# Kernel tuning notes

Measured on AMD Instinct MI355X. Metric: run time of the kernel, lower is better.

The kernel has to match this reference:

```python
import jax, jax.numpy as jnp
import numpy as np

N_EMBED = 1024
N_HEADS = 16
HEAD = N_EMBED // N_HEADS
EPS = 1e-5


def setup_inputs() -> dict:
    key = jax.random.key(0)
    ks = jax.random.split(key, 16)
    C = N_EMBED
    s = lambda fan_in: 1.0 / np.sqrt(fan_in)
    return {
        "x": jax.random.normal(ks[0], (4, 2048, C), jnp.float32),
        "ln1_g": jnp.ones((C,), jnp.float32),
        "ln1_b": jnp.zeros((C,), jnp.float32),
        "w_attn": jax.random.normal(ks[1], (C, 3 * C), jnp.float32) * s(C),
        "b_attn": jnp.zeros((3 * C,), jnp.float32),
        "w_proj": jax.random.normal(ks[2], (C, C), jnp.float32) * s(C),
        "b_proj": jnp.zeros((C,), jnp.float32),
        "ln2_g": jnp.ones((C,), jnp.float32),
        "ln2_b": jnp.zeros((C,), jnp.float32),
        "w_fc": jax.random.normal(ks[3], (C, 4 * C), jnp.float32) * s(C),
        "b_fc": jnp.zeros((4 * C,), jnp.float32),
        "w_fc2": jax.random.normal(ks[4], (4 * C, C), jnp.float32) * s(4 * C),
        "b_fc2": jnp.zeros((C,), jnp.float32),
    }


def _layernorm(x, g, b):
    mu = jnp.mean(x, axis=-1, keepdims=True)
    var = jnp.mean(jnp.square(x - mu), axis=-1, keepdims=True)
    return (x - mu) * jax.lax.rsqrt(var + EPS) * g + b


def _attention(x, w_attn, b_attn, w_proj, b_proj):
    B, T, C = x.shape
    qkv = x @ w_attn + b_attn  # [B,T,3C]
    q, k, v = jnp.split(qkv, 3, axis=-1)
    q = q.reshape(B, T, N_HEADS, HEAD).transpose(0, 2, 1, 3)  # [B,H,T,D]
    k = k.reshape(B, T, N_HEADS, HEAD).transpose(0, 2, 1, 3)
    v = v.reshape(B, T, N_HEADS, HEAD).transpose(0, 2, 1, 3)
    scale = 1.0 / np.sqrt(HEAD)
    affin = jnp.einsum("bhqd,bhkd->bhqk", q, k) * scale  # [B,H,T,T]
    causal = jnp.tril(jnp.ones((T, T), bool))
    affin = jnp.where(causal, affin, -jnp.inf)
    affin = jax.nn.softmax(affin, axis=-1)
    y = jnp.einsum("bhqk,bhkd->bhqd", affin, v)  # [B,H,T,D]
    y = y.transpose(0, 2, 1, 3).reshape(B, T, C)
    return y @ w_proj + b_proj


def reference(x, ln1_g, ln1_b, w_attn, b_attn, w_proj, b_proj,
              ln2_g, ln2_b, w_fc, b_fc, w_fc2, b_fc2):
    x = x + _attention(_layernorm(x, ln1_g, ln1_b), w_attn, b_attn, w_proj, b_proj)
    h = _layernorm(x, ln2_g, ln2_b)
    h = jax.nn.gelu(h @ w_fc + b_fc, approximate=True)  # tanh GELU
    x = x + (h @ w_fc2 + b_fc2)
    return x
```

## Files before the change

### kernel.cpp

```cpp
#include <hip/hip_runtime.h>
#include <math.h>


#define M_ROWS 8192
#define T_SEQ 2048
#define N_EMB 1024
#define N_HEADS 16
#define HEAD_D 64

typedef _Float16 f16;
typedef __attribute__((ext_vector_type(8))) _Float16 f16x8;
typedef __attribute__((ext_vector_type(4))) _Float16 f16x4;
typedef __attribute__((ext_vector_type(4))) float f32x4;

__device__ __forceinline__ void async16(void* lds, const void* g) {
    __builtin_amdgcn_global_load_lds(
        (const __attribute__((address_space(1))) unsigned int*)g,
        (__attribute__((address_space(3))) unsigned int*)lds, 16, 0, 0);
}

__device__ __forceinline__ float gelu_tanh(float v) {
    float u = 0.7978845608028654f * (v + 0.044715f * v * v * v);
    float e = __expf(2.0f * u);
    float t = 1.0f - 2.0f / (e + 1.0f);
    return 0.5f * v * (1.0f + t);
}

__launch_bounds__(256)
__global__ void wconv_kernel(const float* __restrict__ W, f16* __restrict__ WT,
                             int K, int N) {
    __shared__ float t[32][33];
    int tx = threadIdx.x & 31, ty = threadIdx.x >> 5;
    int n0 = blockIdx.x * 32, k0 = blockIdx.y * 32;
    #pragma unroll
    for (int r = 0; r < 4; r++)
        t[ty * 4 + r][tx] = W[(size_t)(k0 + ty * 4 + r) * N + n0 + tx];
    __syncthreads();
    #pragma unroll
    for (int r = 0; r < 4; r++)
        WT[(size_t)(n0 + ty * 4 + r) * K + k0 + tx] = (f16)t[tx][ty * 4 + r];
}

__launch_bounds__(256)
__global__ void ln_kernel(const float* __restrict__ x, const float* __restrict__ g,
                          const float* __restrict__ b, f16* __restrict__ y) {
    int row = blockIdx.x;
    int tid = threadIdx.x;
    const float* xr = x + (size_t)row * N_EMB;
    float4 v = *(const float4*)(xr + tid * 4);
    float s  = v.x + v.y + v.z + v.w;
    float sq = v.x * v.x + v.y * v.y + v.z * v.z + v.w * v.w;
    #pragma unroll
    for (int off = 32; off > 0; off >>= 1) {
        s  += __shfl_down(s, off);
        sq += __shfl_down(sq, off);
    }
    __shared__ float ws_[4], wq_[4];
    __shared__ float mean_s, rstd_s;
    int lane = tid & 63, wid = tid >> 6;
    if (lane == 0) { ws_[wid] = s; wq_[wid] = sq; }
    __syncthreads();
    if (tid == 0) {
        float st = ws_[0] + ws_[1] + ws_[2] + ws_[3];
        float qt = wq_[0] + wq_[1] + wq_[2] + wq_[3];
        float mu = st * (1.0f / N_EMB);
        float var = qt * (1.0f / N_EMB) - mu * mu;
        mean_s = mu;
        rstd_s = rsqrtf(var + 1e-5f);
    }
    __syncthreads();
    float mu = mean_s, r = rstd_s;
    float4 gv = *(const float4*)(g + tid * 4);
    float4 bv = *(const float4*)(b + tid * 4);
    f16x4 o;
    o.x = (f16)((v.x - mu) * r * gv.x + bv.x);
    o.y = (f16)((v.y - mu) * r * gv.y + bv.y);
    o.z = (f16)((v.z - mu) * r * gv.z + bv.z);
    o.w = (f16)((v.w - mu) * r * gv.w + bv.w);
    *(f16x4*)(y + (size_t)row * N_EMB + tid * 4) = o;
}

template <int EPI>
__launch_bounds__(256)
__global__ void gemm_f16(const f16* __restrict__ A, const f16* __restrict__ Bt,
                         const float* __restrict__ bias, const float* __restrict__ res,
                         float* __restrict__ Cf, f16* __restrict__ Ch,
                         f16* __restrict__ vT, int K, int N) {
    __shared__ f16 As[2][128 * 32];
    __shared__ f16 Bs[2][128 * 32];
    int tid = threadIdx.x;
    int lane = tid & 63, wave = tid >> 6;
    int wr = wave >> 1, wc = wave & 1;
    int quad = lane >> 4, l16 = lane & 15;
    int m0 = blockIdx.y * 128, n0 = blockIdx.x * 128;

    int r0 = tid >> 2;
    int s0 = (tid & 3) * 8;
    const f16* paA0 = A  + (size_t)(m0 + r0) * K + s0;
    const f16* paA1 = A  + (size_t)(m0 + r0 + 64) * K + s0;
    const f16* paB0 = Bt + (size_t)(n0 + r0) * K + s0;
    const f16* paB1 = Bt + (size_t)(n0 + r0 + 64) * K + s0;
    char* dA0 = (char*)As + (size_t)tid * 16;
    char* dA1 = (char*)As + (size_t)(256 + tid) * 16;
    char* dB0 = (char*)Bs + (size_t)tid * 16;
    char* dB1 = (char*)Bs + (size_t)(256 + tid) * 16;

    async16(dA0, paA0);
    async16(dA1, paA1);
    async16(dB0, paB0);
    async16(dB1, paB1);

    f32x4 acc[4][4] = {};
    int p = 0;
    for (int k0 = 0; k0 < K; k0 += 32, p ^= 1) {
        __syncthreads();
        if (k0 + 32 < K) {
            int koff = k0 + 32;
            async16(dA0 + (p ^ 1) * 8192, paA0 + koff);
            async16(dA1 + (p ^ 1) * 8192, paA1 + koff);
            async16(dB0 + (p ^ 1) * 8192, paB0 + koff);
            async16(dB1 + (p ^ 1) * 8192, paB1 + koff);
        }
        const f16* as = As[p];
        const f16* bs = Bs[p];
        f16x8 af[4], bf[4];
        #pragma unroll
        for (int i = 0; i < 4; i++)
            af[i] = *(const f16x8*)&as[(wr * 64 + i * 16 + l16) * 32 + quad * 8];
        #pragma unroll
        for (int j = 0; j < 4; j++)
            bf[j] = *(const f16x8*)&bs[(wc * 64 + j * 16 + l16) * 32 + quad * 8];
        #pragma unroll
        for (int i = 0; i < 4; i++)
            #pragma unroll
            for (int j = 0; j < 4; j++)
                acc[i][j] = __builtin_amdgcn_mfma_f32_16x16x32_f16(
                    af[i], bf[j], acc[i][j], 0, 0, 0);
    }

    #pragma unroll
    for (int i = 0; i < 4; i++) {
        int row0 = m0 + wr * 64 + i * 16 + quad * 4;
        #pragma unroll
        for (int j = 0; j < 4; j++) {
            int col = n0 + wc * 64 + j * 16 + l16;
            float bb = bias[col];
            if (EPI == 3) {
                if (n0 < 2048) {
                    #pragma unroll
                    for (int r = 0; r < 4; r++)
                        Ch[(size_t)(row0 + r) * 2048 + col] = (f16)(acc[i][j][r] + bb);
                } else {
                    int hh = (col - 2048) >> 6, dd = col & 63;
                    int bb_ = row0 >> 11, t0 = row0 & 2047;
                    f16x4 pk;
                    pk.x = (f16)(acc[i][j][0] + bb);
                    pk.y = (f16)(acc[i][j][1] + bb);
                    pk.z = (f16)(acc[i][j][2] + bb);
                    pk.w = (f16)(acc[i][j][3] + bb);
                    *(f16x4*)(vT + ((size_t)(bb_ * 16 + hh) * 64 + dd) * 2048 + t0) = pk;
                }
            } else {
                #pragma unroll
                for (int r = 0; r < 4; r++) {
                    size_t idx = (size_t)(row0 + r) * N + col;
                    float v = acc[i][j][r] + bb;
                    if (EPI == 1) v += res[idx];
                    if (EPI == 2) Ch[idx] = (f16)gelu_tanh(v);
                    else          Cf[idx] = v;
                }
            }
        }
    }
}

__launch_bounds__(256, 2)
__global__ void flash_kernel(const f16* __restrict__ qk, const f16* __restrict__ vT,
                             f16* __restrict__ y) {
    __shared__ __align__(16) char smem[67584];
    f16* Ks = (f16*)smem;
    f16* Vs = (f16*)(smem + 16384);
    int tid = threadIdx.x;
    int lane = tid & 63, w = tid >> 6;
    int quad = lane >> 4, l16 = lane & 15;
    f16* Ps = (f16*)(smem + 32768 + w * 8704);

    int bh = blockIdx.y;
    int b = bh >> 4, h = bh & 15;

    for (int half = 0; half < 2; half++) {
        int qt = half ? (int)blockIdx.x : 15 - (int)blockIdx.x;
        int q0 = qt * 128;

        f16x8 qf[2][2];
        #pragma unroll
        for (int qn = 0; qn < 2; qn++) {
            int q = q0 + w * 32 + qn * 16 + l16;
            #pragma unroll
            for (int dblk = 0; dblk < 2; dblk++) {
                f16x8 t = *(const f16x8*)(qk + (size_t)(b * T_SEQ + q) * 2048 +
                                          h * 64 + dblk * 32 + quad * 8);
                #pragma unroll
                for (int e = 0; e < 8; e++) t[e] = t[e] * (f16)0.125f;
                qf[qn][dblk] = t;
            }
        }

        float m_r[2] = {-INFINITY, -INFINITY};
        float l_r[2] = {0.0f, 0.0f};
        f32x4 Oacc[2][4] = {};

        for (int jt = 0; jt <= qt; jt++) {
            int j0 = jt * 128;
            __syncthreads();
            #pragma unroll
            for (int i = 0; i < 4; i++) {
                int L = i * 256 + tid;
                int j = L >> 3, g1 = L & 7;
                int g = g1 ^ (j & 7);
                async16((char*)Ks + (size_t)L * 16,
                        qk + (size_t)(b * T_SEQ + j0 + j) * 2048 + 1024 + h * 64 + g * 8);
            }
            #pragma unroll
            for (int i = 0; i < 4; i++) {
                int L = i * 256 + tid;
                int d = L >> 4, g1 = L & 15;
                int g = (g1 & 8) | ((g1 ^ d) & 7);
                async16((char*)Vs + (size_t)L * 16,
                        vT + ((size_t)(bh) * 64 + d) * 2048 + j0 + g * 8);
            }
            __syncthreads();

            f32x4 S[8][2];
            #pragma unroll
            for (int jm = 0; jm < 8; jm++) {
                f16x8 kf[2];
                #pragma unroll
                for (int dblk = 0; dblk < 2; dblk++) {
                    int j = jm * 16 + l16;
                    int g = (dblk * 4 + quad) ^ (j & 7);
                    kf[dblk] = *(const f16x8*)(Ks + (size_t)(j * 8 + g) * 8);
                }
                #pragma unroll
                for (int qn = 0; qn < 2; qn++) {
                    f32x4 s = {};
                    s = __builtin_amdgcn_mfma_f32_16x16x32_f16(kf[0], qf[qn][0], s, 0, 0, 0);
                    s = __builtin_amdgcn_mfma_f32_16x16x32_f16(kf[1], qf[qn][1], s, 0, 0, 0);
                    S[jm][qn] = s;
                }
            }

            if (jt == qt) {
                #pragma unroll
                for (int jm = 0; jm < 8; jm++)
                    #pragma unroll
                    for (int qn = 0; qn < 2; qn++)
                        #pragma unroll
                        for (int r = 0; r < 4; r++) {
                            int jl = jm * 16 + quad * 4 + r;
                            int ql = w * 32 + qn * 16 + l16;
                            if (jl > ql) S[jm][qn][r] = -1e30f;
                        }
            }

            float alpha[2];
            #pragma unroll
            for (int qn = 0; qn < 2; qn++) {
                float tmax = -INFINITY;
                #pragma unroll
                for (int jm = 0; jm < 8; jm++)
                    #pragma unroll
                    for (int r = 0; r < 4; r++)
                        tmax = fmaxf(tmax, S[jm][qn][r]);
                tmax = fmaxf(tmax, __shfl_xor(tmax, 16));
                tmax = fmaxf(tmax, __shfl_xor(tmax, 32));
                float mnew = fmaxf(m_r[qn], tmax);
                alpha[qn] = __expf(m_r[qn] - mnew);
                m_r[qn] = mnew;
                float rsum = 0.0f;
                #pragma unroll
                for (int jm = 0; jm < 8; jm++)
                    #pragma unroll
                    for (int r = 0; r < 4; r++) {
                        float p = __expf(S[jm][qn][r] - mnew);
                        S[jm][qn][r] = p;
                        rsum += p;
                    }
                rsum += __shfl_xor(rsum, 16);
                rsum += __shfl_xor(rsum, 32);
                l_r[qn] = l_r[qn] * alpha[qn] + rsum;
            }

            #pragma unroll
            for (int jm = 0; jm < 8; jm++)
                #pragma unroll
                for (int qn = 0; qn < 2; qn++) {
                    f16x4 pk;
                    pk.x = (f16)S[jm][qn][0];
                    pk.y = (f16)S[jm][qn][1];
                    pk.z = (f16)S[jm][qn][2];
                    pk.w = (f16)S[jm][qn][3];
                    *(f16x4*)(Ps + (size_t)(qn * 16 + l16) * 136 + jm * 16 + quad * 4) = pk;
                }

            float aPV[2][4];
            #pragma unroll
            for (int m = 0; m < 2; m++)
                #pragma unroll
                for (int r = 0; r < 4; r++)
                    aPV[m][r] = __shfl(alpha[m], quad * 20 + r);
            #pragma unroll
            for (int m = 0; m < 2; m++)
                #pragma unroll
                for (int n = 0; n < 4; n++)
                    #pragma unroll
                    for (int r = 0; r < 4; r++)
                        Oacc[m][n][r] *= aPV[m][r];

            #pragma unroll
            for (int kblk = 0; kblk < 4; kblk++) {
                f16x8 pf[2];
                #pragma unroll
                for (int m = 0; m < 2; m++)
                    pf[m] = *(const f16x8*)(Ps + (size_t)(m * 16 + l16) * 136 +
                                            kblk * 32 + quad * 8);
                f16x8 vf[4];
                #pragma unroll
                for (int n = 0; n < 4; n++) {
                    int d = n * 16 + l16;
                    int g = (kblk * 4 + quad);
                    int gs = (g & 8) | ((g ^ d) & 7);
                    vf[n] = *(const f16x8*)(Vs + (size_t)(d * 16 + gs) * 8);
                }
                #pragma unroll
                for (int m = 0; m < 2; m++)
                    #pragma unroll
                    for (int n = 0; n < 4; n++)
                        Oacc[m][n] = __builtin_amdgcn_mfma_f32_16x16x32_f16(
                            pf[m], vf[n], Oacc[m][n], 0, 0, 0);
            }
        }

        #pragma unroll
        for (int m = 0; m < 2; m++) {
            float lPV[4];
            #pragma unroll
            for (int r = 0; r < 4; r++)
                lPV[r] = 1.0f / __shfl(l_r[m], quad * 20 + r);
            #pragma unroll
            for (int n = 0; n < 4; n++) {
                #pragma unroll
                for (int r = 0; r < 4; r++) {
                    int q = q0 + w * 32 + m * 16 + quad * 4 + r;
                    y[(size_t)(b * T_SEQ + q) * N_EMB + h * 64 + n * 16 + l16] =
                        (f16)(Oacc[m][n][r] * lPV[r]);
                }
            }
        }
    }
}

extern "C" void kernel_launch(void* const* d_in, const int* in_sizes, int n_in,
                              void* d_out, int out_size, void* d_ws, size_t ws_size,
                              hipStream_t stream) {
    const float* x      = (const float*)d_in[0];
    const float* ln1_g  = (const float*)d_in[1];
    const float* ln1_b  = (const float*)d_in[2];
    const float* w_attn = (const float*)d_in[3];
    const float* b_attn = (const float*)d_in[4];
    const float* w_proj = (const float*)d_in[5];
    const float* b_proj = (const float*)d_in[6];
    const float* ln2_g  = (const float*)d_in[7];
    const float* ln2_b  = (const float*)d_in[8];
    const float* w_fc   = (const float*)d_in[9];
    const float* b_fc   = (const float*)d_in[10];
    const float* w_fc2  = (const float*)d_in[11];
    const float* b_fc2  = (const float*)d_in[12];
    float* out = (float*)d_out;

    const size_t MB = 1024 * 1024;
    char* ws = (char*)d_ws;
    f16*   lnbuf = (f16*)ws;
    f16*   qkbuf = (f16*)(ws + 16 * MB);
    f16*   vTbuf = (f16*)(ws + 48 * MB);
    f16*   ybuf  = (f16*)(ws + 64 * MB);
    f16*   h     = (f16*)(ws + 80 * MB);
    f16*   wT    = (f16*)(ws + 144 * MB);
    f16* wT_attn = wT;
    f16* wT_proj = wT_attn + (size_t)3072 * 1024;
    f16* wT_fc   = wT_proj + (size_t)1024 * 1024;
    f16* wT_fc2  = wT_fc   + (size_t)1024 * 4096;

    wconv_kernel<<<dim3(3072 / 32, 1024 / 32), 256, 0, stream>>>(w_attn, wT_attn, 1024, 3072);
    wconv_kernel<<<dim3(1024 / 32, 1024 / 32), 256, 0, stream>>>(w_proj, wT_proj, 1024, 1024);
    wconv_kernel<<<dim3(4096 / 32, 1024 / 32), 256, 0, stream>>>(w_fc,   wT_fc,   1024, 4096);
    wconv_kernel<<<dim3(1024 / 32, 4096 / 32), 256, 0, stream>>>(w_fc2,  wT_fc2,  4096, 1024);

    ln_kernel<<<M_ROWS, 256, 0, stream>>>(x, ln1_g, ln1_b, lnbuf);
    gemm_f16<3><<<dim3(3072 / 128, M_ROWS / 128), 256, 0, stream>>>(
        lnbuf, wT_attn, b_attn, nullptr, nullptr, qkbuf, vTbuf, 1024, 3072);
    flash_kernel<<<dim3(8, 64), 256, 0, stream>>>(qkbuf, vTbuf, ybuf);
    gemm_f16<1><<<dim3(1024 / 128, M_ROWS / 128), 256, 0, stream>>>(
        ybuf, wT_proj, b_proj, x, out, nullptr, nullptr, 1024, 1024);
    ln_kernel<<<M_ROWS, 256, 0, stream>>>(out, ln2_g, ln2_b, lnbuf);
    gemm_f16<2><<<dim3(4096 / 128, M_ROWS / 128), 256, 0, stream>>>(
        lnbuf, wT_fc, b_fc, nullptr, nullptr, h, nullptr, 1024, 4096);
    gemm_f16<1><<<dim3(1024 / 128, M_ROWS / 128), 256, 0, stream>>>(
        h, wT_fc2, b_fc2, out, out, nullptr, nullptr, 4096, 1024);
}
```

Baseline: 525.3 us.

## Triple-buffer GEMM LDS pipeline with explicit vmcnt waits and XCD tile swizzle

The GEMM main loop moves from a double-buffered async global-to-LDS prefetch to a three-stage ring. Explicit s_waitcnt vmcnt values let two tiles stay in flight while the current one is consumed, and barriers now sit on both sides of the compute. Workgroup IDs are remapped so that consecutive tiles land on the same XCD for L2 reuse, and s_setprio raises wave priority during the MFMA block. The swizzle assumes the workgroup count is divisible by 8, and the extra LDS buffer plus second barrier may lower occupancy.

```diff
diff --git a/kernel.cpp b/kernel.cpp
--- a/kernel.cpp
+++ b/kernel.cpp
@@ -86,13 +86,19 @@
                          const float* __restrict__ bias, const float* __restrict__ res,
                          float* __restrict__ Cf, f16* __restrict__ Ch,
                          f16* __restrict__ vT, int K, int N) {
-    __shared__ f16 As[2][128 * 32];
-    __shared__ f16 Bs[2][128 * 32];
+    __shared__ f16 As[3][128 * 32];
+    __shared__ f16 Bs[3][128 * 32];
     int tid = threadIdx.x;
     int lane = tid & 63, wave = tid >> 6;
     int wr = wave >> 1, wc = wave & 1;
     int quad = lane >> 4, l16 = lane & 15;
-    int m0 = blockIdx.y * 128, n0 = blockIdx.x * 128;
+
+    int nx = gridDim.x;
+    int nwg = nx * gridDim.y;
+    int orig = blockIdx.y * nx + blockIdx.x;
+    int cpx = nwg >> 3;
+    int swz = (orig & 7) * cpx + (orig >> 3);
+    int m0 = (swz / nx) * 128, n0 = (swz % nx) * 128;
 
     int r0 = tid >> 2;
     int s0 = (tid & 3) * 8;
@@ -100,29 +106,39 @@
     const f16* paA1 = A  + (size_t)(m0 + r0 + 64) * K + s0;
     const f16* paB0 = Bt + (size_t)(n0 + r0) * K + s0;
     const f16* paB1 = Bt + (size_t)(n0 + r0 + 64) * K + s0;
-    char* dA0 = (char*)As + (size_t)tid * 16;
-    char* dA1 = (char*)As + (size_t)(256 + tid) * 16;
-    char* dB0 = (char*)Bs + (size_t)tid * 16;
-    char* dB1 = (char*)Bs + (size_t)(256 + tid) * 16;
-
-    async16(dA0, paA0);
-    async16(dA1, paA1);
-    async16(dB0, paB0);
-    async16(dB1, paB1);
+    char* sA0 = (char*)As + (size_t)tid * 16;
+    char* sA1 = (char*)As + (size_t)(256 + tid) * 16;
+    char* sB0 = (char*)Bs + (size_t)tid * 16;
+    char* sB1 = (char*)Bs + (size_t)(256 + tid) * 16;
+
+    int nt = K >> 5;
+
+    {
+        async16(sA0, paA0); async16(sA1, paA1);
+        async16(sB0, paB0); async16(sB1, paB1);
+        async16(sA0 + 8192, paA0 + 32); async16(sA1 + 8192, paA1 + 32);
+        async16(sB0 + 8192, paB0 + 32); async16(sB1 + 8192, paB1 + 32);
+    }
 
     f32x4 acc[4][4] = {};
-    int p = 0;
-    for (int k0 = 0; k0 < K; k0 += 32, p ^= 1) {
-        __syncthreads();
-        if (k0 + 32 < K) {
-            int koff = k0 + 32;
-            async16(dA0 + (p ^ 1) * 8192, paA0 + koff);
-            async16(dA1 + (p ^ 1) * 8192, paA1 + koff);
-            async16(dB0 + (p ^ 1) * 8192, paB0 + koff);
-            async16(dB1 + (p ^ 1) * 8192, paB1 + koff);
+    int bc = 0;
+    for (int t = 0; t < nt; t++) {
+        if (t + 2 < nt) {
+            int b2 = bc ? bc - 1 : 2;
+            size_t bo = (size_t)b2 * 8192;
+            int koff = (t + 2) * 32;
+            async16(sA0 + bo, paA0 + koff); async16(sA1 + bo, paA1 + koff);
+            async16(sB0 + bo, paB0 + koff); async16(sB1 + bo, paB1 + koff);
+            asm volatile("s_waitcnt vmcnt(8)" ::: "memory");
+        } else if (t + 2 == nt) {
+            asm volatile("s_waitcnt vmcnt(4)" ::: "memory");
+        } else {
+            asm volatile("s_waitcnt vmcnt(0)" ::: "memory");
         }
-        const f16* as = As[p];
-        const f16* bs = Bs[p];
+        __builtin_amdgcn_s_barrier();
+
+        const f16* as = As[bc];
+        const f16* bs = Bs[bc];
         f16x8 af[4], bf[4];
         #pragma unroll
         for (int i = 0; i < 4; i++)
@@ -130,12 +146,16 @@
         #pragma unroll
         for (int j = 0; j < 4; j++)
             bf[j] = *(const f16x8*)&bs[(wc * 64 + j * 16 + l16) * 32 + quad * 8];
+        __builtin_amdgcn_s_setprio(1);
         #pragma unroll
         for (int i = 0; i < 4; i++)
             #pragma unroll
             for (int j = 0; j < 4; j++)
                 acc[i][j] = __builtin_amdgcn_mfma_f32_16x16x32_f16(
                     af[i], bf[j], acc[i][j], 0, 0, 0);
+        __builtin_amdgcn_s_setprio(0);
+        __builtin_amdgcn_s_barrier();
+        bc = (bc == 2) ? 0 : bc + 1;
     }
 
     #pragma unroll
```

After: 523.7 us. No clear change (-0.3%).
